# Kernel tuning notes

Measured on AMD Instinct MI355X. Metric: run time of the kernel, lower is better.

## Reference

```python
import jax, jax.numpy as jnp
import numpy as np

# ---- geometry / discretization constants (match init_kwargs) ----
IMG_H, IMG_W = 512, 512
N_VIEWS = 180
N_DET = 512
DET_SPACING = 2.0
VOXEL_SPACING = 1.0
SID = 600.0          # source-to-isocenter distance
IDD = 500.0          # isocenter-to-detector distance
N_SAMPLES = 512      # ray-marching samples per ray (Joseph-style)


def _bilinear(img, px, py):
    """Bilinear sample of 2D image at pixel coords (px=cols, py=rows); 0 outside."""
    H, W = img.shape
    ix0 = jnp.floor(px)
    iy0 = jnp.floor(py)
    fx = px - ix0
    fy = py - iy0
    ix0 = ix0.astype(jnp.int32)
    iy0 = iy0.astype(jnp.int32)
    ix1 = ix0 + 1
    iy1 = iy0 + 1
    flat = img.reshape(-1)

    def gather(iy, ix):
        valid = (ix >= 0) & (ix < W) & (iy >= 0) & (iy < H)
        idx = jnp.clip(iy, 0, H - 1) * W + jnp.clip(ix, 0, W - 1)
        return jnp.where(valid, jnp.take(flat, idx), 0.0)

    return (gather(iy0, ix0) * (1.0 - fx) * (1.0 - fy)
            + gather(iy0, ix1) * fx * (1.0 - fy)
            + gather(iy1, ix0) * (1.0 - fx) * fy
            + gather(iy1, ix1) * fx * fy)


def fan_project(img, src_pos, det_center, det_u_vec):
    """Fan-beam forward projection: line integrals src -> each detector bin.
    img: [H,W]; src_pos/det_center/det_u_vec: [V,2]. Returns sinogram [V,n_det]."""
    H, W = img.shape
    # detector bin offsets along the detector tangent, centered
    u = (jnp.arange(N_DET, dtype=img.dtype) - (N_DET - 1) / 2.0) * DET_SPACING  # [D]
    det_pts = det_center[:, None, :] + u[None, :, None] * det_u_vec[:, None, :]  # [V,D,2]
    src = src_pos[:, None, :]                                                    # [V,1,2]
    d = det_pts - src                                                            # [V,D,2]
    seg_len = jnp.sqrt(d[..., 0] ** 2 + d[..., 1] ** 2)                          # [V,D]
    # midpoint samples t in (0,1) along each ray
    t = (jnp.arange(N_SAMPLES, dtype=img.dtype) + 0.5) / N_SAMPLES               # [S]
    pts_x = src[..., 0][:, :, None] + t[None, None, :] * d[..., 0][:, :, None]   # [V,D,S]
    pts_y = src[..., 1][:, :, None] + t[None, None, :] * d[..., 1][:, :, None]   # [V,D,S]
    # world -> pixel coords (image centered at origin)
    px = pts_x / VOXEL_SPACING + (W - 1) / 2.0
    py = pts_y / VOXEL_SPACING + (H - 1) / 2.0
    vals = _bilinear(img, px, py)                                                # [V,D,S]
    return vals.sum(axis=-1) * (seg_len / N_SAMPLES)                             # [V,D]


def setup_inputs() -> dict:
    key = jax.random.key(0)
    k1, k2 = jax.random.split(key)
    x = jax.random.normal(k1, (IMG_H, IMG_W), dtype=jnp.float32)
    reco = jax.random.normal(k2, (IMG_H, IMG_W), dtype=jnp.float32) * 0.01
    ang = np.linspace(0.0, 2.0 * np.pi, N_VIEWS, endpoint=False).astype(np.float32)
    cos_a, sin_a = np.cos(ang), np.sin(ang)
    src_pos = jnp.asarray(np.stack([SID * cos_a, SID * sin_a], axis=-1))
    det_center = jnp.asarray(np.stack([-IDD * cos_a, -IDD * sin_a], axis=-1))
    det_u_vec = jnp.asarray(np.stack([-sin_a, cos_a], axis=-1))
    return {"x": x, "reco": reco, "src_pos": src_pos,
            "det_center": det_center, "det_u_vec": det_u_vec}


def reference(x, reco, src_pos, det_center, det_u_vec):
    updated = x + reco
    sino = fan_project(updated, src_pos, det_center, det_u_vec)
    return sino, jax.nn.relu(updated)
```

## Files before the change

### kernel.cpp

```cpp
#include <hip/hip_runtime.h>
#include <hip/hip_bf16.h>
#include <hip/hip_fp16.h>

#define IMG_H 512
#define IMG_W 512
#define N_VIEWS 180
#define N_DET 512
#define N_SAMPLES 512

#define N_RAYS (N_VIEWS * N_DET)
#define IMG_N (IMG_H * IMG_W)

#define QPAD 8
#define QDIM (IMG_W + 1 + 2 * QPAD)
#define R_N (QDIM * QDIM)
#define R_BYTES ((size_t)R_N * 4)
#define R_BYTES_AL ((R_BYTES + 255) & ~(size_t)255)
#define RAYINFO_BYTES ((size_t)N_RAYS * 32)

#define K_CHUNKS 4
#define PACK_BLOCKS ((R_N + 255) / 256)
#define SETUP_BLOCKS (N_RAYS / 256)

__global__ __launch_bounds__(256) void prep_kernel(
        const float* __restrict__ x, const float* __restrict__ r,
        unsigned* __restrict__ Rrm, unsigned* __restrict__ Tcm,
        float* __restrict__ relu_out,
        const float* __restrict__ src_pos,
        const float* __restrict__ det_center,
        const float* __restrict__ det_u,
        float4* __restrict__ RA, float4* __restrict__ RB,
        float* __restrict__ sino) {
    const int b = blockIdx.x;
    if (b < PACK_BLOCKS) {
        int i = b * 256 + threadIdx.x;
        if (i >= R_N) return;
        int row = i / QDIM;
        int col = i - row * QDIM;
        int yy = row - QPAD;
        int xx = col - QPAD;
        float v0 = 0.f, v1 = 0.f;
        if ((unsigned)xx < (unsigned)IMG_W) {
            if ((unsigned)yy < (unsigned)IMG_H) {
                int idx = yy * IMG_W + xx;
                v0 = x[idx] + r[idx];
            }
            if ((unsigned)(yy + 1) < (unsigned)IMG_H) {
                int idx = (yy + 1) * IMG_W + xx;
                v1 = x[idx] + r[idx];
            }
        }
        __half2 h = __floats2half2_rn(v0, v1);
        Rrm[i] = *reinterpret_cast<unsigned*>(&h);
        if ((unsigned)xx < (unsigned)IMG_W && (unsigned)yy < (unsigned)IMG_H)
            relu_out[yy * IMG_W + xx] = fmaxf(v0, 0.f);
        return;
    }
    if (b < 2 * PACK_BLOCKS) {
        int j = (b - PACK_BLOCKS) * 256 + threadIdx.x;
        if (j >= R_N) return;
        int row = j / QDIM;
        int col = j - row * QDIM;
        int rp = row - QPAD;
        int cp = col - QPAD;
        float v0 = 0.f, v1 = 0.f;
        if ((unsigned)cp < (unsigned)IMG_H) {
            int base = cp * IMG_W;
            if ((unsigned)rp < (unsigned)IMG_W)       v0 = x[base + rp] + r[base + rp];
            if ((unsigned)(rp + 1) < (unsigned)IMG_W) v1 = x[base + rp + 1] + r[base + rp + 1];
        }
        __half2 h = __floats2half2_rn(v0, v1);
        Tcm[j] = *reinterpret_cast<unsigned*>(&h);
        return;
    }

    const int rid = (b - 2 * PACK_BLOCKS) * 256 + threadIdx.x;
    const int v   = rid >> 9;
    const int det = rid & 511;

    float sx = src_pos[2 * v];
    float sy = src_pos[2 * v + 1];
    const float ux = det_u[2 * v];
    const float uy = det_u[2 * v + 1];
    const float u  = ((float)det - 255.5f) * 2.0f;
    float ex = det_center[2 * v]     + u * ux;
    float ey = det_center[2 * v + 1] + u * uy;

    const bool useT = fabsf(uy) > fabsf(ux);
    if (useT) {
        float tmp = sx; sx = sy; sy = tmp;
        tmp = ex; ex = ey; ey = tmp;
    }

    const float dx = ex - sx;
    const float dy = ey - sy;
    const float segscl = sqrtf(dx * dx + dy * dy) * (1.0f / (float)N_SAMPLES);

    const float lo = -256.5f, hi = 256.5f;
    float t0 = 0.f, t1 = 1.f;
    if (fabsf(dx) > 1e-12f) {
        float ta = (lo - sx) / dx, tb = (hi - sx) / dx;
        t0 = fmaxf(t0, fminf(ta, tb));
        t1 = fminf(t1, fmaxf(ta, tb));
    } else if (sx <= lo || sx >= hi) {
        t1 = -1.f;
    }
    if (fabsf(dy) > 1e-12f) {
        float ta = (lo - sy) / dy, tb = (hi - sy) / dy;
        t0 = fmaxf(t0, fminf(ta, tb));
        t1 = fminf(t1, fmaxf(ta, tb));
    } else if (sy <= lo || sy >= hi) {
        t1 = -1.f;
    }
    int s0 = 0, len = 0;
    if (t1 >= t0) {
        s0 = max(0, (int)floorf(t0 * (float)N_SAMPLES - 0.5f) - 1);
        int s1 = min(N_SAMPLES - 1, (int)ceilf(t1 * (float)N_SAMPLES - 0.5f) + 1);
        len = s1 - s0 + 1;
        if (len < 0) len = 0;
    }
    RA[rid] = make_float4(dx, dy, sx + 255.5f + (float)QPAD,
                                  sy + 255.5f + (float)QPAD);
    RB[rid] = make_float4(segscl, (float)s0, (float)len, useT ? 1.f : 0.f);
    sino[rid] = 0.f;
}

__device__ __forceinline__ float sample_h(const unsigned* __restrict__ R,
                                          float t, float dx, float dy,
                                          float bx, float by, float acc) {
    const float px = fmaf(t, dx, bx);
    const float py = fmaf(t, dy, by);
    const float ixf = truncf(px);
    const float iyf = truncf(py);
    const float fx = px - ixf;
    const float fy = py - iyf;
    const float linf = fmaf(iyf, (float)QDIM, ixf);
    const int lin = (int)linf;

    uint2 qw;
    __builtin_memcpy(&qw, R + lin, 8);
    const float2 fa = __half22float2(*reinterpret_cast<const __half2*>(&qw.x));
    const float2 fb = __half22float2(*reinterpret_cast<const __half2*>(&qw.y));

    const float gx = 1.f - fx;
    const float h0 = fmaf(fx, fb.x, gx * fa.x);
    const float h1 = fmaf(fx, fb.y, gx * fa.y);
    acc = fmaf(1.f - fy, h0, acc);
    acc = fmaf(fy, h1, acc);
    return acc;
}

__global__ __launch_bounds__(256) void fanproj_tile_kernel(
        const unsigned* __restrict__ Rrm, const unsigned* __restrict__ Tcm,
        const float4* __restrict__ RA, const float4* __restrict__ RB,
        float* __restrict__ sino) {
    const int tix  = threadIdx.x;
    const int lane = tix & 63;
    const int dsub = lane & 15;
    const int soff = lane >> 4;
    const int rid  = blockIdx.x * 64 + ((tix >> 6) << 4) + dsub;
    const int chunk = blockIdx.y;

    const float4 a = RA[rid];
    const float4 b = RB[rid];
    const float dx = a.x, dy = a.y, bx = a.z, by = a.w;
    const int s0  = (int)b.y;
    const int len = (int)b.z;
    const unsigned* __restrict__ R = (b.w != 0.f) ? Tcm : Rrm;
    const int c0 = s0 + ((len * chunk) >> 2);
    const int c1 = s0 + ((len * (chunk + 1)) >> 2) - 1;

    int s = c0 + soff;
    float t = ((float)s + 0.5f) * (1.0f / (float)N_SAMPLES);
    float acc0 = 0.f, acc1 = 0.f, acc2 = 0.f, acc3 = 0.f;
    for (; s + 12 <= c1; s += 16) {
        acc0 = sample_h(R, t,               dx, dy, bx, by, acc0);
        acc1 = sample_h(R, t + 0.0078125f,  dx, dy, bx, by, acc1);
        acc2 = sample_h(R, t + 0.015625f,   dx, dy, bx, by, acc2);
        acc3 = sample_h(R, t + 0.0234375f,  dx, dy, bx, by, acc3);
        t += 0.03125f;
    }
    for (; s <= c1; s += 4) {
        acc0 = sample_h(R, t, dx, dy, bx, by, acc0);
        t += 0.0078125f;
    }

    float acc = (acc0 + acc1) + (acc2 + acc3);
    acc += __shfl_xor(acc, 16);
    acc += __shfl_xor(acc, 32);
    if (soff == 0) {
        const float res = acc * b.x;
        if (res != 0.f) atomicAdd(&sino[rid], res);
    }
}

__global__ __launch_bounds__(256) void add_kernel(const float4* __restrict__ x,
                                                  const float4* __restrict__ r,
                                                  float4* __restrict__ upd) {
    int i = blockIdx.x * blockDim.x + threadIdx.x;
    float4 a = x[i];
    float4 b = r[i];
    upd[i] = make_float4(a.x + b.x, a.y + b.y, a.z + b.z, a.w + b.w);
}
__global__ __launch_bounds__(256) void relu_kernel(const float4* __restrict__ upd,
                                                   float4* __restrict__ out) {
    int i = blockIdx.x * blockDim.x + threadIdx.x;
    float4 c = upd[i];
    out[i] = make_float4(fmaxf(c.x, 0.f), fmaxf(c.y, 0.f),
                         fmaxf(c.z, 0.f), fmaxf(c.w, 0.f));
}

__device__ __forceinline__ float sample_plain(const float* __restrict__ img,
                                              int s, float dx, float dy,
                                              float bx, float by, float acc) {
    const float t  = fmaf((float)s, 1.f / (float)N_SAMPLES,
                          0.5f / (float)N_SAMPLES);
    const float px = fmaf(t, dx, bx);
    const float py = fmaf(t, dy, by);
    const float ix0f = floorf(px);
    const float iy0f = floorf(py);
    const float fx = px - ix0f;
    const float fy = py - iy0f;
    const int ix0 = (int)ix0f;
    const int iy0 = (int)iy0f;
    const float gx = ((unsigned)ix0       < (unsigned)IMG_W) ? (1.f - fx) : 0.f;
    const float hx = ((unsigned)(ix0 + 1) < (unsigned)IMG_W) ? fx         : 0.f;
    const float gy = ((unsigned)iy0       < (unsigned)IMG_H) ? (1.f - fy) : 0.f;
    const float hy = ((unsigned)(iy0 + 1) < (unsigned)IMG_H) ? fy         : 0.f;
    const unsigned cx0 = (unsigned)min(max(ix0, 0), IMG_W - 1);
    const unsigned cx1 = (unsigned)min(max(ix0 + 1, 0), IMG_W - 1);
    const unsigned r0  = (unsigned)min(max(iy0, 0), IMG_H - 1) << 9;
    const unsigned r1  = (unsigned)min(max(iy0 + 1, 0), IMG_H - 1) << 9;
    const float v00 = img[r0 + cx0];
    const float v01 = img[r0 + cx1];
    const float v10 = img[r1 + cx0];
    const float v11 = img[r1 + cx1];
    acc = fmaf(v00, gx * gy, acc);
    acc = fmaf(v01, hx * gy, acc);
    acc = fmaf(v10, gx * hy, acc);
    acc = fmaf(v11, hx * hy, acc);
    return acc;
}

__global__ __launch_bounds__(256) void fanproj_plain_kernel(
        const float* __restrict__ img,
        const float* __restrict__ src_pos,
        const float* __restrict__ det_center,
        const float* __restrict__ det_u,
        float* __restrict__ sino) {
    const int wid  = (blockIdx.x * blockDim.x + threadIdx.x) >> 6;
    const int lane = threadIdx.x & 63;
    if (wid >= N_RAYS) return;
    const int v   = wid >> 9;
    const int det = wid & 511;
    const float sx = src_pos[2 * v];
    const float sy = src_pos[2 * v + 1];
    const float u  = ((float)det - 255.5f) * 2.0f;
    const float ex = det_center[2 * v]     + u * det_u[2 * v];
    const float ey = det_center[2 * v + 1] + u * det_u[2 * v + 1];
    const float dx = ex - sx;
    const float dy = ey - sy;
    const float seg = sqrtf(dx * dx + dy * dy);
    const float bx = sx + 255.5f;
    const float by = sy + 255.5f;
    const float lo = -256.5f, hi = 256.5f;
    float t0 = 0.f, t1 = 1.f;
    if (fabsf(dx) > 1e-12f) {
        float ta = (lo - sx) / dx, tb = (hi - sx) / dx;
        t0 = fmaxf(t0, fminf(ta, tb));
        t1 = fminf(t1, fmaxf(ta, tb));
    } else if (sx <= lo || sx >= hi) {
        t1 = -1.f;
    }
    if (fabsf(dy) > 1e-12f) {
        float ta = (lo - sy) / dy, tb = (hi - sy) / dy;
        t0 = fmaxf(t0, fminf(ta, tb));
        t1 = fminf(t1, fmaxf(ta, tb));
    } else if (sy <= lo || sy >= hi) {
        t1 = -1.f;
    }
    int s0 = 0, s1 = -1;
    if (t1 >= t0) {
        s0 = max(0, (int)floorf(t0 * (float)N_SAMPLES - 0.5f) - 1);
        s1 = min(N_SAMPLES - 1, (int)ceilf(t1 * (float)N_SAMPLES - 0.5f) + 1);
    }
    float acc0 = 0.f, acc1 = 0.f;
    int s = s0 + lane;
    for (; s + 64 <= s1; s += 128) {
        acc0 = sample_plain(img, s,      dx, dy, bx, by, acc0);
        acc1 = sample_plain(img, s + 64, dx, dy, bx, by, acc1);
    }
    if (s <= s1) acc0 = sample_plain(img, s, dx, dy, bx, by, acc0);
    float acc = acc0 + acc1;
    #pragma unroll
    for (int off = 32; off >= 1; off >>= 1) acc += __shfl_xor(acc, off);
    if (lane == 0) sino[wid] = acc * seg * (1.0f / (float)N_SAMPLES);
}

extern "C" void kernel_launch(void* const* d_in, const int* in_sizes, int n_in,
                              void* d_out, int out_size, void* d_ws, size_t ws_size,
                              hipStream_t stream) {
    const float* x          = (const float*)d_in[0];
    const float* reco       = (const float*)d_in[1];
    const float* src_pos    = (const float*)d_in[2];
    const float* det_center = (const float*)d_in[3];
    const float* det_u      = (const float*)d_in[4];

    float* out  = (float*)d_out;
    float* sino = out;
    float* relu = out + N_RAYS;

    const int n4 = IMG_N / 4;

    if (ws_size >= 2 * R_BYTES_AL + RAYINFO_BYTES) {
        unsigned* Rrm = (unsigned*)d_ws;
        unsigned* Tcm = (unsigned*)((char*)d_ws + R_BYTES_AL);
        float4*   RA  = (float4*)((char*)d_ws + 2 * R_BYTES_AL);
        float4*   RB  = RA + N_RAYS;
        prep_kernel<<<2 * PACK_BLOCKS + SETUP_BLOCKS, 256, 0, stream>>>(
            x, reco, Rrm, Tcm, relu, src_pos, det_center, det_u, RA, RB, sino);
        fanproj_tile_kernel<<<dim3(N_RAYS / 64, K_CHUNKS), 256, 0, stream>>>(
            Rrm, Tcm, RA, RB, sino);
    } else {
        float* upd = relu;
        add_kernel<<<n4 / 256, 256, 0, stream>>>(
            (const float4*)x, (const float4*)reco, (float4*)upd);
        fanproj_plain_kernel<<<N_RAYS / 4, 256, 0, stream>>>(
            upd, src_pos, det_center, det_u, sino);
        relu_kernel<<<n4 / 256, 256, 0, stream>>>(
            (const float4*)upd, (float4*)relu);
    }
}
```

Baseline: 38.00 us.

## Stage image row bands in LDS and project each view per band

Replaces the global-memory gather projection kernel with a band kernel. Each block copies a 33-row band of the packed half-precision image into shared memory and handles all 512 detectors of one view, sampling only the ray segment that crosses that band. Partial sums are combined with atomics across the 16 bands. This is meant to turn scattered global/L2 gathers into LDS reads. In exchange it adds per-band LDS fill cost (about 68KB per block), limits occupancy, puts more atomics on each ray and adds branchy per-sample band checks.

Result: slower. 45.46 us (+19.6%).

```diff
diff --git a/kernel.cpp b/kernel.cpp
--- a/kernel.cpp
+++ b/kernel.cpp
@@ -18,7 +18,11 @@
 #define R_BYTES_AL ((R_BYTES + 255) & ~(size_t)255)
 #define RAYINFO_BYTES ((size_t)N_RAYS * 32)
 
-#define K_CHUNKS 4
+#define BROWS 33
+#define NBANDS 16
+#define LDSN (BROWS * QDIM)
+#define LDS_BYTES (LDSN * 4)
+
 #define PACK_BLOCKS ((R_N + 255) / 256)
 #define SETUP_BLOCKS (N_RAYS / 256)
 
@@ -91,7 +95,6 @@
         float tmp = sx; sx = sy; sy = tmp;
         tmp = ex; ex = ey; ey = tmp;
     }
-
     const float dx = ex - sx;
     const float dy = ey - sy;
     const float segscl = sqrtf(dx * dx + dy * dy) * (1.0f / (float)N_SAMPLES);
@@ -121,76 +124,125 @@
     }
     RA[rid] = make_float4(dx, dy, sx + 255.5f + (float)QPAD,
                                   sy + 255.5f + (float)QPAD);
-    RB[rid] = make_float4(segscl, (float)s0, (float)len, useT ? 1.f : 0.f);
+    RB[rid] = make_float4(segscl, (float)s0, (float)len,
+                          (float)N_SAMPLES / dy);
     sino[rid] = 0.f;
 }
 
-__device__ __forceinline__ float sample_h(const unsigned* __restrict__ R,
-                                          float t, float dx, float dy,
-                                          float bx, float by, float acc) {
-    const float px = fmaf(t, dx, bx);
-    const float py = fmaf(t, dy, by);
-    const float ixf = truncf(px);
-    const float iyf = truncf(py);
-    const float fx = px - ixf;
-    const float fy = py - iyf;
-    const float linf = fmaf(iyf, (float)QDIM, ixf);
-    const int lin = (int)linf;
-
-    uint2 qw;
-    __builtin_memcpy(&qw, R + lin, 8);
-    const float2 fa = __half22float2(*reinterpret_cast<const __half2*>(&qw.x));
-    const float2 fb = __half22float2(*reinterpret_cast<const __half2*>(&qw.y));
-
-    const float gx = 1.f - fx;
-    const float h0 = fmaf(fx, fb.x, gx * fa.x);
-    const float h1 = fmaf(fx, fb.y, gx * fa.y);
-    acc = fmaf(1.f - fy, h0, acc);
-    acc = fmaf(fy, h1, acc);
-    return acc;
-}
-
-__global__ __launch_bounds__(256) void fanproj_tile_kernel(
+__global__ __launch_bounds__(1024, 8) void fanproj_band_kernel(
         const unsigned* __restrict__ Rrm, const unsigned* __restrict__ Tcm,
+        const float* __restrict__ det_u,
         const float4* __restrict__ RA, const float4* __restrict__ RB,
         float* __restrict__ sino) {
-    const int tix  = threadIdx.x;
-    const int lane = tix & 63;
-    const int dsub = lane & 15;
-    const int soff = lane >> 4;
-    const int rid  = blockIdx.x * 64 + ((tix >> 6) << 4) + dsub;
-    const int chunk = blockIdx.y;
+    extern __shared__ unsigned lds[];
+    const int band = blockIdx.x;
+    const int v    = blockIdx.y;
+    const int tid  = threadIdx.x;
+
+    const bool useT = fabsf(det_u[2 * v + 1]) > fabsf(det_u[2 * v]);
+    const unsigned* __restrict__ src = (useT ? Tcm : Rrm) + band * LDSN;
+
+    for (int j = tid; j < LDSN / 4; j += 1024) {
+        uint4 q;
+        __builtin_memcpy(&q, src + 4 * j, 16);
+        *reinterpret_cast<uint4*>(&lds[4 * j]) = q;
+    }
+    if (tid == 0) lds[LDSN - 1] = src[LDSN - 1];
+    __syncthreads();
+
+    const int det  = tid >> 1;
+    const int soff = tid & 1;
+    const int rid  = (v << 9) | det;
 
     const float4 a = RA[rid];
     const float4 b = RB[rid];
     const float dx = a.x, dy = a.y, bx = a.z, by = a.w;
-    const int s0  = (int)b.y;
-    const int len = (int)b.z;
-    const unsigned* __restrict__ R = (b.w != 0.f) ? Tcm : Rrm;
-    const int c0 = s0 + ((len * chunk) >> 2);
-    const int c1 = s0 + ((len * (chunk + 1)) >> 2) - 1;
-
-    int s = c0 + soff;
+    const int   s0 = (int)b.y;
+    const int   len = (int)b.z;
+    const float invstep = b.w;
+
+    const float B0f = (float)(band * BROWS);
+    const float step = dy * (1.0f / (float)N_SAMPLES);
+    const float start = by + 0.5f * step;
+
+    float loF = (B0f - start) * invstep;
+    float hiF = (B0f + (float)BROWS - start) * invstep;
+    if (invstep < 0.f) { float tmp = loF; loF = hiF; hiF = tmp; }
+    const int sb0 = max(s0, (int)floorf(loF) - 1);
+    const int sb1 = min(s0 + len - 1, (int)ceilf(hiF) + 1);
+
+    int s = sb0 + soff;
     float t = ((float)s + 0.5f) * (1.0f / (float)N_SAMPLES);
-    float acc0 = 0.f, acc1 = 0.f, acc2 = 0.f, acc3 = 0.f;
-    for (; s + 12 <= c1; s += 16) {
-        acc0 = sample_h(R, t,               dx, dy, bx, by, acc0);
-        acc1 = sample_h(R, t + 0.0078125f,  dx, dy, bx, by, acc1);
-        acc2 = sample_h(R, t + 0.015625f,   dx, dy, bx, by, acc2);
-        acc3 = sample_h(R, t + 0.0234375f,  dx, dy, bx, by, acc3);
-        t += 0.03125f;
-    }
-    for (; s <= c1; s += 4) {
-        acc0 = sample_h(R, t, dx, dy, bx, by, acc0);
+    float acc0 = 0.f, acc1 = 0.f;
+    for (; s + 2 <= sb1; s += 4) {
+        {
+            const float px = fmaf(t, dx, bx);
+            const float pyr = fmaf(t, dy, by) - B0f;
+            if (pyr >= 0.f && pyr < (float)BROWS) {
+                const float ixf = truncf(px);
+                const float iylf = truncf(pyr);
+                const float fx = px - ixf;
+                const float fy = pyr - iylf;
+                const int lin = (int)fmaf(iylf, (float)QDIM, ixf);
+                uint2 qw;
+                __builtin_memcpy(&qw, &lds[lin], 8);
+                const float2 fa = __half22float2(*reinterpret_cast<const __half2*>(&qw.x));
+                const float2 fb = __half22float2(*reinterpret_cast<const __half2*>(&qw.y));
+                const float gx = 1.f - fx;
+                const float h0 = fmaf(fx, fb.x, gx * fa.x);
+                const float h1 = fmaf(fx, fb.y, gx * fa.y);
+                acc0 = fmaf(1.f - fy, h0, acc0);
+                acc0 = fmaf(fy, h1, acc0);
+            }
+        }
+        {
+            const float t2 = t + 0.00390625f;
+            const float px = fmaf(t2, dx, bx);
+            const float pyr = fmaf(t2, dy, by) - B0f;
+            if (pyr >= 0.f && pyr < (float)BROWS) {
+                const float ixf = truncf(px);
+                const float iylf = truncf(pyr);
+                const float fx = px - ixf;
+                const float fy = pyr - iylf;
+                const int lin = (int)fmaf(iylf, (float)QDIM, ixf);
+                uint2 qw;
+                __builtin_memcpy(&qw, &lds[lin], 8);
+                const float2 fa = __half22float2(*reinterpret_cast<const __half2*>(&qw.x));
+                const float2 fb = __half22float2(*reinterpret_cast<const __half2*>(&qw.y));
+                const float gx = 1.f - fx;
+                const float h0 = fmaf(fx, fb.x, gx * fa.x);
+                const float h1 = fmaf(fx, fb.y, gx * fa.y);
+                acc1 = fmaf(1.f - fy, h0, acc1);
+                acc1 = fmaf(fy, h1, acc1);
+            }
+        }
         t += 0.0078125f;
     }
-
-    float acc = (acc0 + acc1) + (acc2 + acc3);
-    acc += __shfl_xor(acc, 16);
-    acc += __shfl_xor(acc, 32);
-    if (soff == 0) {
-        const float res = acc * b.x;
-        if (res != 0.f) atomicAdd(&sino[rid], res);
+    if (s <= sb1) {
+        const float px = fmaf(t, dx, bx);
+        const float pyr = fmaf(t, dy, by) - B0f;
+        if (pyr >= 0.f && pyr < (float)BROWS) {
+            const float ixf = truncf(px);
+            const float iylf = truncf(pyr);
+            const float fx = px - ixf;
+            const float fy = pyr - iylf;
+            const int lin = (int)fmaf(iylf, (float)QDIM, ixf);
+            uint2 qw;
+            __builtin_memcpy(&qw, &lds[lin], 8);
+            const float2 fa = __half22float2(*reinterpret_cast<const __half2*>(&qw.x));
+            const float2 fb = __half22float2(*reinterpret_cast<const __half2*>(&qw.y));
+            const float gx = 1.f - fx;
+            const float h0 = fmaf(fx, fb.x, gx * fa.x);
+            const float h1 = fmaf(fx, fb.y, gx * fa.y);
+            acc0 = fmaf(1.f - fy, h0, acc0);
+            acc0 = fmaf(fy, h1, acc0);
+        }
+    }
+
+    float acc = acc0 + acc1;
+    acc += __shfl_xor(acc, 1);
+    if (soff == 0 && acc != 0.f) {
+        atomicAdd(&sino[rid], acc * b.x);
     }
 }
 
@@ -319,8 +371,8 @@
         float4*   RB  = RA + N_RAYS;
         prep_kernel<<<2 * PACK_BLOCKS + SETUP_BLOCKS, 256, 0, stream>>>(
             x, reco, Rrm, Tcm, relu, src_pos, det_center, det_u, RA, RB, sino);
-        fanproj_tile_kernel<<<dim3(N_RAYS / 64, K_CHUNKS), 256, 0, stream>>>(
-            Rrm, Tcm, RA, RB, sino);
+        fanproj_band_kernel<<<dim3(NBANDS, N_VIEWS), 1024, LDS_BYTES, stream>>>(
+            Rrm, Tcm, det_u, RA, RB, sino);
     } else {
         float* upd = relu;
         add_kernel<<<n4 / 256, 256, 0, stream>>>(
```
